# Performance work log

Hardware: AMD Instinct MI355X
Metric: run time of the kernel (lower is better)

Reference implementation:

```python
import jax, jax.numpy as jnp
import numpy as np

H, HD = 8, 32            # num_heads, head_dim
OUT = H * HD             # out_channels = 256
NUM_GRAPHS = 1


def segment_softmax(logits, seg, num_segments):
    m = jax.ops.segment_max(logits, seg, num_segments=num_segments)
    m = jnp.where(jnp.isfinite(m), m, 0.0)
    e = jnp.exp(logits - m[seg])
    s = jax.ops.segment_sum(e, seg, num_segments=num_segments)
    return e / (s[seg] + 1e-16)


def setup_inputs():
    key = jax.random.key(0)
    ks = jax.random.split(key, 16)
    N, E, IN = 30000, 600000, 128
    s = 0.05
    return {
        "x": jax.random.normal(ks[0], (N, IN), jnp.float32),
        "edge_index": jax.random.randint(ks[1], (2, E), 0, N, jnp.int32),
        "edge_attr": jax.random.normal(ks[2], (E,), jnp.float32),
        "batch": jnp.zeros((N,), jnp.int32),
        # per-head GATConv params (stacked over heads)
        "W": jax.random.normal(ks[3], (H, IN, HD), jnp.float32) * s,
        "a_src": jax.random.normal(ks[4], (H, HD), jnp.float32) * s,
        "a_dst": jax.random.normal(ks[5], (H, HD), jnp.float32) * s,
        "conv_b": jnp.zeros((H, HD), jnp.float32),
        # shared fc (used twice in forward)
        "fc_w": jax.random.normal(ks[6], (OUT, OUT), jnp.float32) * s,
        "fc_b": jnp.zeros((OUT,), jnp.float32),
        "ln_w": jnp.ones((OUT,), jnp.float32),
        "ln_b": jnp.zeros((OUT,), jnp.float32),
        "gate_w": jax.random.normal(ks[7], (1, OUT), jnp.float32) * s,
        "gate_b": jnp.zeros((1,), jnp.float32),
        "gfc_w": jax.random.normal(ks[8], (OUT, OUT), jnp.float32) * s,
        "gfc_b": jnp.zeros((OUT,), jnp.float32),
    }


def reference(x, edge_index, edge_attr, batch, W, a_src, a_dst, conv_b,
              fc_w, fc_b, ln_w, ln_b, gate_w, gate_b, gfc_w, gfc_b):
    N = x.shape[0]
    # (dropout p=0.2 is identity in eval mode)
    # --- multi-head GATConv (heads=1 each, vectorized over H); PyG default
    # add_self_loops=True; edge_dim=None so edge_attr is ignored by the conv.
    loops = jnp.arange(N, dtype=edge_index.dtype)
    src = jnp.concatenate([edge_index[0], loops])  # [Etot]
    dst = jnp.concatenate([edge_index[1], loops])
    xp = jnp.einsum('ni,hid->nhd', x, W)                    # [N,H,HD]
    alpha_src = jnp.sum(xp * a_src[None], axis=-1)          # [N,H]
    alpha_dst = jnp.sum(xp * a_dst[None], axis=-1)          # [N,H]
    logits = jax.nn.leaky_relu(alpha_src[src] + alpha_dst[dst], 0.2)  # [Etot,H]
    alpha = segment_softmax(logits, dst, N)                 # [Etot,H]
    msg = alpha[:, :, None] * xp[src]                        # [Etot,H,HD]
    out = jax.ops.segment_sum(msg, dst, num_segments=N) + conv_b[None]
    x_local = out.reshape(N, OUT)                            # concat over heads
    # --- dense re-attention / softmax fusion
    sa = jax.nn.softmax(jax.nn.leaky_relu(x_local @ fc_w.T + fc_b, 0.01), axis=-1)
    x_local = jax.nn.leaky_relu(x_local * sa, 0.2)
    x_local = x_local @ fc_w.T + fc_b
    # LayerNorm (eps=1e-5)
    mu = jnp.mean(x_local, axis=-1, keepdims=True)
    var = jnp.mean(jnp.square(x_local - mu), axis=-1, keepdims=True)
    x_local = (x_local - mu) / jnp.sqrt(var + 1e-5) * ln_w + ln_b
    # F.normalize(p=2, dim=1)
    nrm = jnp.sqrt(jnp.sum(jnp.square(x_local), axis=1, keepdims=True))
    x_local = x_local / jnp.maximum(nrm, 1e-12)
    # --- GlobalAttention pooling
    gate = (x_local @ gate_w.T + gate_b)[:, 0]               # [N]
    g = segment_softmax(gate, batch, NUM_GRAPHS)             # [N]
    x_global = jax.ops.segment_sum(g[:, None] * x_local, batch,
                                   num_segments=NUM_GRAPHS)  # [1,OUT]
    ga = jax.nn.softmax(jax.nn.relu(x_global @ gfc_w.T + gfc_b), axis=-1)
    return x_local * ga[batch]                               # [N,OUT]
```

## Files before the change

kernel.cpp:

```cpp
#include <hip/hip_runtime.h>


#define PAD 96

typedef __attribute__((ext_vector_type(8))) short bf16x8;
typedef __attribute__((ext_vector_type(4))) float f32x4;

__device__ __forceinline__ float leaky_f(float v, float s) { return v > 0.f ? v : s * v; }
__device__ __forceinline__ unsigned short f2bf(float f) {
  unsigned int u = __float_as_uint(f);
  u += 0x7fffu + ((u >> 16) & 1u);
  return (unsigned short)(u >> 16);
}
__device__ __forceinline__ float bf2f(unsigned short u) {
  return __uint_as_float(((unsigned int)u) << 16);
}
__device__ __forceinline__ float red16_sum(float v) {
#pragma unroll
  for (int m = 1; m < 16; m <<= 1) v += __shfl_xor(v, m);
  return v;
}
__device__ __forceinline__ float red16_max(float v) {
#pragma unroll
  for (int m = 1; m < 16; m <<= 1) v = fmaxf(v, __shfl_xor(v, m));
  return v;
}

__global__ void repack_zero_kernel(const float* __restrict__ W, const float* __restrict__ fc_w,
                                   const float* __restrict__ gfc_w,
                                   unsigned short* __restrict__ Wb,
                                   unsigned short* __restrict__ fcB, float* __restrict__ gfcT,
                                   int* __restrict__ count, int n) {
  int i = blockIdx.x * 256 + threadIdx.x;
  if (i < 256 * 128) {
    int c = i >> 7, k = i & 127;
    Wb[i] = f2bf(W[((c >> 5) * 128 + k) * 32 + (c & 31)]);
  } else if (i < 256 * 128 + 256 * 256) {
    int j = i - 256 * 128;
    fcB[j] = f2bf(fc_w[j]);
  } else if (i < 256 * 128 + 2 * 256 * 256) {
    int j = i - 256 * 128 - 256 * 256;
    gfcT[j] = gfc_w[(j & 255) * 256 + (j >> 8)];
  }
  if (i < n) count[i] = 0;
}

__global__ __launch_bounds__(256) void scatter_kernel(
    const int* __restrict__ esrc, const int* __restrict__ edst,
    int* __restrict__ count, int* __restrict__ ssrc, int E) {
  int base = (blockIdx.x * 256 + threadIdx.x) * 4;
  if (base + 4 <= E) {
    int4 d4 = *(const int4*)(edst + base);
    int4 s4 = *(const int4*)(esrc + base);
    int p0 = atomicAdd(&count[d4.x], 1);
    int p1 = atomicAdd(&count[d4.y], 1);
    int p2 = atomicAdd(&count[d4.z], 1);
    int p3 = atomicAdd(&count[d4.w], 1);
    if (p0 < PAD) ssrc[(size_t)d4.x * PAD + p0] = s4.x;
    if (p1 < PAD) ssrc[(size_t)d4.y * PAD + p1] = s4.y;
    if (p2 < PAD) ssrc[(size_t)d4.z * PAD + p2] = s4.z;
    if (p3 < PAD) ssrc[(size_t)d4.w * PAD + p3] = s4.w;
  } else {
    for (int i = base; i < E; ++i) {
      int d = edst[i];
      int p = atomicAdd(&count[d], 1);
      if (p < PAD) ssrc[(size_t)d * PAD + p] = esrc[i];
    }
  }
}

template <int A_BF16>
__device__ __forceinline__ void gemm_body_64x256(
    const void* __restrict__ Av, const unsigned short* __restrict__ B,
    int row0, int n_rows, int K, short As[64][72], short Bs[256][72],
    f32x4 acc[4][4]) {
  int t = threadIdx.x;
  int wave = t >> 6, lane = t & 63;
  int m16 = lane & 15, quad = lane >> 4;
  int wc = wave * 64;
  for (int k0 = 0; k0 < K; k0 += 64) {
    if (A_BF16) {
      const unsigned short* A = (const unsigned short*)Av;
#pragma unroll
      for (int p = 0; p < 2; ++p) {
        int e = (p * 256 + t) * 8;
        int row = e >> 6, k = e & 63;
        int ar = row0 + row; if (ar > n_rows - 1) ar = n_rows - 1;
        uint4 q = *(const uint4*)(A + (size_t)ar * K + k0 + k);
        *(uint4*)&As[row][k] = q;
      }
    } else {
      const float* A = (const float*)Av;
#pragma unroll
      for (int p = 0; p < 4; ++p) {
        int e = (p * 256 + t) * 4;
        int row = e >> 6, k = e & 63;
        int ar = row0 + row; if (ar > n_rows - 1) ar = n_rows - 1;
        float4 q = *(const float4*)(A + (size_t)ar * K + k0 + k);
        unsigned int lo = (unsigned int)f2bf(q.x) | ((unsigned int)f2bf(q.y) << 16);
        unsigned int hi = (unsigned int)f2bf(q.z) | ((unsigned int)f2bf(q.w) << 16);
        *(uint2*)&As[row][k] = make_uint2(lo, hi);
      }
    }
#pragma unroll
    for (int p = 0; p < 8; ++p) {
      int e = (p * 256 + t) * 8;
      int nn = e >> 6, k = e & 63;
      uint4 q = *(const uint4*)(B + (size_t)nn * K + k0 + k);
      *(uint4*)&Bs[nn][k] = q;
    }
    __syncthreads();
#pragma unroll
    for (int ks = 0; ks < 64; ks += 32) {
      bf16x8 af[4], bfr[4];
#pragma unroll
      for (int i = 0; i < 4; ++i)
        af[i] = *(const bf16x8*)&As[i * 16 + m16][ks + quad * 8];
#pragma unroll
      for (int j = 0; j < 4; ++j)
        bfr[j] = *(const bf16x8*)&Bs[wc + j * 16 + m16][ks + quad * 8];
#pragma unroll
      for (int i = 0; i < 4; ++i)
#pragma unroll
        for (int j = 0; j < 4; ++j)
          acc[i][j] = __builtin_amdgcn_mfma_f32_16x16x32_bf16(af[i], bfr[j], acc[i][j], 0, 0, 0);
    }
    __syncthreads();
  }
}

__global__ __launch_bounds__(256) void gemm_xp(
    const float* __restrict__ A, const unsigned short* __restrict__ B,
    const float* __restrict__ a_src, const float* __restrict__ a_dst,
    unsigned short* __restrict__ xpb, float* __restrict__ asrc,
    float* __restrict__ adst, int n_rows) {
  __shared__ short As[64][72];
  __shared__ short Bs[256][72];
  int t = threadIdx.x;
  int wave = t >> 6, lane = t & 63;
  int m16 = lane & 15, quad = lane >> 4;
  int wc = wave * 64;
  int row0 = blockIdx.x * 64;
  f32x4 acc[4][4];
#pragma unroll
  for (int i = 0; i < 4; ++i)
#pragma unroll
    for (int j = 0; j < 4; ++j) acc[i][j] = (f32x4){0.f, 0.f, 0.f, 0.f};
  gemm_body_64x256<0>(A, B, row0, n_rows, 128, As, Bs, acc);

  float av[4], bd[4];
#pragma unroll
  for (int j = 0; j < 4; ++j) {
    int c = wc + j * 16 + m16;
    av[j] = a_src[c];
    bd[j] = a_dst[c];
  }
#pragma unroll
  for (int i = 0; i < 4; ++i)
#pragma unroll
    for (int v = 0; v < 4; ++v) {
      int r = row0 + i * 16 + quad * 4 + v;
      if (r < n_rows) {
#pragma unroll
        for (int j = 0; j < 4; ++j)
          xpb[(size_t)r * 256 + wc + j * 16 + m16] = f2bf(acc[i][j][v]);
      }
      float s0 = acc[i][0][v] * av[0] + acc[i][1][v] * av[1];
      float s1 = acc[i][2][v] * av[2] + acc[i][3][v] * av[3];
      float d0 = acc[i][0][v] * bd[0] + acc[i][1][v] * bd[1];
      float d1 = acc[i][2][v] * bd[2] + acc[i][3][v] * bd[3];
      s0 = red16_sum(s0); s1 = red16_sum(s1);
      d0 = red16_sum(d0); d1 = red16_sum(d1);
      if (m16 == 0 && r < n_rows) {
        asrc[(size_t)r * 8 + 2 * wave] = s0;
        asrc[(size_t)r * 8 + 2 * wave + 1] = s1;
        adst[(size_t)r * 8 + 2 * wave] = d0;
        adst[(size_t)r * 8 + 2 * wave + 1] = d1;
      }
    }
}

__global__ __launch_bounds__(256) void gemm_sm(
    const float* __restrict__ A, const unsigned short* __restrict__ B,
    const float* __restrict__ bias, unsigned short* __restrict__ x2b, int n_rows) {
  __shared__ short As[64][72];
  __shared__ short Bs[256][72];
  __shared__ float red[4][64];
  __shared__ float rowv[64];
  int t = threadIdx.x;
  int wave = t >> 6, lane = t & 63;
  int m16 = lane & 15, quad = lane >> 4;
  int wc = wave * 64;
  int row0 = blockIdx.x * 64;
  f32x4 acc[4][4];
#pragma unroll
  for (int i = 0; i < 4; ++i)
#pragma unroll
    for (int j = 0; j < 4; ++j) acc[i][j] = (f32x4){0.f, 0.f, 0.f, 0.f};
  gemm_body_64x256<0>(A, B, row0, n_rows, 256, As, Bs, acc);

  float bvv[4];
#pragma unroll
  for (int j = 0; j < 4; ++j) bvv[j] = bias[wc + j * 16 + m16];
#pragma unroll
  for (int i = 0; i < 4; ++i)
#pragma unroll
    for (int j = 0; j < 4; ++j)
#pragma unroll
      for (int v = 0; v < 4; ++v)
        acc[i][j][v] = leaky_f(acc[i][j][v] + bvv[j], 0.01f);

  float M[4][4];
#pragma unroll
  for (int i = 0; i < 4; ++i)
#pragma unroll
    for (int v = 0; v < 4; ++v) {
      float m = fmaxf(fmaxf(acc[i][0][v], acc[i][1][v]), fmaxf(acc[i][2][v], acc[i][3][v]));
      M[i][v] = red16_max(m);
    }
  if (m16 == 0)
#pragma unroll
    for (int i = 0; i < 4; ++i)
#pragma unroll
      for (int v = 0; v < 4; ++v) red[wave][i * 16 + quad * 4 + v] = M[i][v];
  __syncthreads();
  if (t < 64) rowv[t] = fmaxf(fmaxf(red[0][t], red[1][t]), fmaxf(red[2][t], red[3][t]));
  __syncthreads();
#pragma unroll
  for (int i = 0; i < 4; ++i)
#pragma unroll
    for (int v = 0; v < 4; ++v) M[i][v] = rowv[i * 16 + quad * 4 + v];
  __syncthreads();

  float S[4][4];
#pragma unroll
  for (int i = 0; i < 4; ++i)
#pragma unroll
    for (int v = 0; v < 4; ++v) {
#pragma unroll
      for (int j = 0; j < 4; ++j) acc[i][j][v] = __expf(acc[i][j][v] - M[i][v]);
      float s = acc[i][0][v] + acc[i][1][v] + acc[i][2][v] + acc[i][3][v];
      S[i][v] = red16_sum(s);
    }
  if (m16 == 0)
#pragma unroll
    for (int i = 0; i < 4; ++i)
#pragma unroll
      for (int v = 0; v < 4; ++v) red[wave][i * 16 + quad * 4 + v] = S[i][v];
  __syncthreads();
  if (t < 64) rowv[t] = red[0][t] + red[1][t] + red[2][t] + red[3][t];
  __syncthreads();

#pragma unroll
  for (int i = 0; i < 4; ++i)
#pragma unroll
    for (int v = 0; v < 4; ++v) {
      int r = row0 + i * 16 + quad * 4 + v;
      float inv = 1.f / rowv[i * 16 + quad * 4 + v];
      if (r < n_rows) {
#pragma unroll
        for (int j = 0; j < 4; ++j) {
          int c = wc + j * 16 + m16;
          float xv = A[(size_t)r * 256 + c];
          x2b[(size_t)r * 256 + c] = f2bf(leaky_f(xv * acc[i][j][v] * inv, 0.2f));
        }
      }
    }
}

__global__ __launch_bounds__(256) void gemm_ln(
    const unsigned short* __restrict__ A, const unsigned short* __restrict__ B,
    const float* __restrict__ bias, const float* __restrict__ ln_w,
    const float* __restrict__ ln_b, const float* __restrict__ gate_w,
    const float* __restrict__ gate_b, unsigned short* __restrict__ Cout,
    float* __restrict__ pooled, float* __restrict__ pooledS, int n_rows) {
  __shared__ short As[64][72];
  __shared__ short Bs[256][72];
  __shared__ float red[4][64];
  __shared__ float rowv[64];
  __shared__ float eg[64];
  int t = threadIdx.x;
  int wave = t >> 6, lane = t & 63;
  int m16 = lane & 15, quad = lane >> 4;
  int wc = wave * 64;
  int row0 = blockIdx.x * 64;
  f32x4 acc[4][4];
#pragma unroll
  for (int i = 0; i < 4; ++i)
#pragma unroll
    for (int j = 0; j < 4; ++j) acc[i][j] = (f32x4){0.f, 0.f, 0.f, 0.f};
  gemm_body_64x256<1>(A, B, row0, n_rows, 256, As, Bs, acc);

  float bvv[4], lw[4], lb[4], gw[4];
#pragma unroll
  for (int j = 0; j < 4; ++j) {
    int c = wc + j * 16 + m16;
    bvv[j] = bias[c]; lw[j] = ln_w[c]; lb[j] = ln_b[c]; gw[j] = gate_w[c];
  }
#pragma unroll
  for (int i = 0; i < 4; ++i)
#pragma unroll
    for (int j = 0; j < 4; ++j)
#pragma unroll
      for (int v = 0; v < 4; ++v) acc[i][j][v] += bvv[j];

  float MU[4][4];
#pragma unroll
  for (int i = 0; i < 4; ++i)
#pragma unroll
    for (int v = 0; v < 4; ++v)
      MU[i][v] = red16_sum(acc[i][0][v] + acc[i][1][v] + acc[i][2][v] + acc[i][3][v]);
  if (m16 == 0)
#pragma unroll
    for (int i = 0; i < 4; ++i)
#pragma unroll
      for (int v = 0; v < 4; ++v) red[wave][i * 16 + quad * 4 + v] = MU[i][v];
  __syncthreads();
  if (t < 64) rowv[t] = (red[0][t] + red[1][t] + red[2][t] + red[3][t]) * (1.f / 256.f);
  __syncthreads();
#pragma unroll
  for (int i = 0; i < 4; ++i)
#pragma unroll
    for (int v = 0; v < 4; ++v) MU[i][v] = rowv[i * 16 + quad * 4 + v];
  __syncthreads();
#pragma unroll
  for (int i = 0; i < 4; ++i)
#pragma unroll
    for (int j = 0; j < 4; ++j)
#pragma unroll
      for (int v = 0; v < 4; ++v) acc[i][j][v] -= MU[i][v];

  float RS[4][4];
#pragma unroll
  for (int i = 0; i < 4; ++i)
#pragma unroll
    for (int v = 0; v < 4; ++v) {
      float q = acc[i][0][v] * acc[i][0][v] + acc[i][1][v] * acc[i][1][v] +
                acc[i][2][v] * acc[i][2][v] + acc[i][3][v] * acc[i][3][v];
      RS[i][v] = red16_sum(q);
    }
  if (m16 == 0)
#pragma unroll
    for (int i = 0; i < 4; ++i)
#pragma unroll
      for (int v = 0; v < 4; ++v) red[wave][i * 16 + quad * 4 + v] = RS[i][v];
  __syncthreads();
  if (t < 64)
    rowv[t] = rsqrtf((red[0][t] + red[1][t] + red[2][t] + red[3][t]) * (1.f / 256.f) + 1e-5f);
  __syncthreads();
#pragma unroll
  for (int i = 0; i < 4; ++i)
#pragma unroll
    for (int v = 0; v < 4; ++v) RS[i][v] = rowv[i * 16 + quad * 4 + v];
  __syncthreads();
#pragma unroll
  for (int i = 0; i < 4; ++i)
#pragma unroll
    for (int j = 0; j < 4; ++j)
#pragma unroll
      for (int v = 0; v < 4; ++v)
        acc[i][j][v] = acc[i][j][v] * RS[i][v] * lw[j] + lb[j];

  float NV[4][4];
#pragma unroll
  for (int i = 0; i < 4; ++i)
#pragma unroll
    for (int v = 0; v < 4; ++v) {
      float q = acc[i][0][v] * acc[i][0][v] + acc[i][1][v] * acc[i][1][v] +
                acc[i][2][v] * acc[i][2][v] + acc[i][3][v] * acc[i][3][v];
      NV[i][v] = red16_sum(q);
    }
  if (m16 == 0)
#pragma unroll
    for (int i = 0; i < 4; ++i)
#pragma unroll
      for (int v = 0; v < 4; ++v) red[wave][i * 16 + quad * 4 + v] = NV[i][v];
  __syncthreads();
  if (t < 64)
    rowv[t] = 1.f / fmaxf(sqrtf(red[0][t] + red[1][t] + red[2][t] + red[3][t]), 1e-12f);
  __syncthreads();
#pragma unroll
  for (int i = 0; i < 4; ++i)
#pragma unroll
    for (int v = 0; v < 4; ++v) NV[i][v] = rowv[i * 16 + quad * 4 + v];
  __syncthreads();
#pragma unroll
  for (int i = 0; i < 4; ++i)
#pragma unroll
    for (int j = 0; j < 4; ++j)
#pragma unroll
      for (int v = 0; v < 4; ++v) acc[i][j][v] *= NV[i][v];

  float GP[4][4];
#pragma unroll
  for (int i = 0; i < 4; ++i)
#pragma unroll
    for (int v = 0; v < 4; ++v) {
      float g = acc[i][0][v] * gw[0] + acc[i][1][v] * gw[1] +
                acc[i][2][v] * gw[2] + acc[i][3][v] * gw[3];
      GP[i][v] = red16_sum(g);
    }
  if (m16 == 0)
#pragma unroll
    for (int i = 0; i < 4; ++i)
#pragma unroll
      for (int v = 0; v < 4; ++v) red[wave][i * 16 + quad * 4 + v] = GP[i][v];
  __syncthreads();
  if (t < 64) {
    float gp = red[0][t] + red[1][t] + red[2][t] + red[3][t];
    float e = (row0 + t < n_rows) ? __expf(gp + gate_b[0]) : 0.f;
    eg[t] = e;
#pragma unroll
    for (int m = 1; m < 64; m <<= 1) e += __shfl_xor(e, m);
    if (t == 0) pooledS[blockIdx.x] = e;
  }
  __syncthreads();

  {
    float pt[4] = {0.f, 0.f, 0.f, 0.f};
#pragma unroll
    for (int i = 0; i < 4; ++i)
#pragma unroll
      for (int v = 0; v < 4; ++v) {
        float w = eg[i * 16 + quad * 4 + v];
#pragma unroll
        for (int j = 0; j < 4; ++j) pt[j] += w * acc[i][j][v];
      }
#pragma unroll
    for (int j = 0; j < 4; ++j) {
      float sj = pt[j];
      sj += __shfl_xor(sj, 16);
      sj += __shfl_xor(sj, 32);
      if (quad == 0) pooled[(size_t)blockIdx.x * 256 + wc + j * 16 + m16] = sj;
    }
  }

#pragma unroll
  for (int i = 0; i < 4; ++i)
#pragma unroll
    for (int v = 0; v < 4; ++v) {
      int r = row0 + i * 16 + quad * 4 + v;
      if (r < n_rows) {
#pragma unroll
        for (int j = 0; j < 4; ++j)
          Cout[(size_t)r * 256 + wc + j * 16 + m16] = f2bf(acc[i][j][v]);
      }
    }
}

__global__ __launch_bounds__(256) void agg_kernel(
    const unsigned short* __restrict__ xpb, const float* __restrict__ asrc,
    const float* __restrict__ adst, const int* __restrict__ count,
    const int* __restrict__ ssrc, const float4* __restrict__ conv_b4,
    float4* __restrict__ xloc4, int n_nodes) {
  int lane = threadIdx.x & 63, w = threadIdx.x >> 6;
  int n = blockIdx.x * 4 + w;
  if (n >= n_nodes) return;
  int h = lane >> 3;
  float ad = adst[n * 8 + h];
  float p = __expf(leaky_f(asrc[n * 8 + h] + ad, 0.2f));
  ushort4 xq = ((const ushort4*)(xpb + (size_t)n * 256))[lane];
  float4 acc;
  acc.x = p * bf2f(xq.x); acc.y = p * bf2f(xq.y);
  acc.z = p * bf2f(xq.z); acc.w = p * bf2f(xq.w);
  float ssum = p;
  int beg = n * PAD;
  int end = beg + count[n];
  int j = beg;
  for (; j + 8 <= end; j += 8) {
    int sv[8];
#pragma unroll
    for (int u = 0; u < 8; ++u) sv[u] = ssrc[j + u];
    float a[8];
#pragma unroll
    for (int u = 0; u < 8; ++u) a[u] = asrc[sv[u] * 8 + h];
    ushort4 q[8];
#pragma unroll
    for (int u = 0; u < 8; ++u) q[u] = ((const ushort4*)(xpb + (size_t)sv[u] * 256))[lane];
#pragma unroll
    for (int u = 0; u < 8; ++u) {
      float pu = __expf(leaky_f(a[u] + ad, 0.2f));
      acc.x += pu * bf2f(q[u].x); acc.y += pu * bf2f(q[u].y);
      acc.z += pu * bf2f(q[u].z); acc.w += pu * bf2f(q[u].w);
      ssum += pu;
    }
  }
  for (; j + 4 <= end; j += 4) {
    int sv0 = ssrc[j], sv1 = ssrc[j + 1], sv2 = ssrc[j + 2], sv3 = ssrc[j + 3];
    float a0 = asrc[sv0 * 8 + h];
    float a1 = asrc[sv1 * 8 + h];
    float a2 = asrc[sv2 * 8 + h];
    float a3 = asrc[sv3 * 8 + h];
    ushort4 q0 = ((const ushort4*)(xpb + (size_t)sv0 * 256))[lane];
    ushort4 q1 = ((const ushort4*)(xpb + (size_t)sv1 * 256))[lane];
    ushort4 q2 = ((const ushort4*)(xpb + (size_t)sv2 * 256))[lane];
    ushort4 q3 = ((const ushort4*)(xpb + (size_t)sv3 * 256))[lane];
    float p0 = __expf(leaky_f(a0 + ad, 0.2f));
    float p1 = __expf(leaky_f(a1 + ad, 0.2f));
    float p2 = __expf(leaky_f(a2 + ad, 0.2f));
    float p3 = __expf(leaky_f(a3 + ad, 0.2f));
    acc.x += p0 * bf2f(q0.x); acc.y += p0 * bf2f(q0.y);
    acc.z += p0 * bf2f(q0.z); acc.w += p0 * bf2f(q0.w);
    acc.x += p1 * bf2f(q1.x); acc.y += p1 * bf2f(q1.y);
    acc.z += p1 * bf2f(q1.z); acc.w += p1 * bf2f(q1.w);
    acc.x += p2 * bf2f(q2.x); acc.y += p2 * bf2f(q2.y);
    acc.z += p2 * bf2f(q2.z); acc.w += p2 * bf2f(q2.w);
    acc.x += p3 * bf2f(q3.x); acc.y += p3 * bf2f(q3.y);
    acc.z += p3 * bf2f(q3.z); acc.w += p3 * bf2f(q3.w);
    ssum += p0 + p1 + p2 + p3;
  }
  for (; j < end; ++j) {
    int sv = ssrc[j];
    float a1 = asrc[sv * 8 + h];
    ushort4 q = ((const ushort4*)(xpb + (size_t)sv * 256))[lane];
    float p1 = __expf(leaky_f(a1 + ad, 0.2f));
    acc.x += p1 * bf2f(q.x); acc.y += p1 * bf2f(q.y);
    acc.z += p1 * bf2f(q.z); acc.w += p1 * bf2f(q.w);
    ssum += p1;
  }
  float inv = 1.f / (ssum + 1e-16f);
  float4 b = conv_b4[lane];
  float4 o;
  o.x = acc.x * inv + b.x; o.y = acc.y * inv + b.y;
  o.z = acc.z * inv + b.z; o.w = acc.w * inv + b.w;
  xloc4[(size_t)n * 64 + lane] = o;
}

__global__ __launch_bounds__(1024) void finalize_gfc(
    const float* __restrict__ pooled, const float* __restrict__ pooledS, int nb,
    const float* __restrict__ gfcT, const float* __restrict__ gfc_b,
    float* __restrict__ ga) {
  __shared__ float sm[1024];
  __shared__ float xs[256];
  __shared__ float av[256];
  int t = threadIdx.x, c = t & 255, part = t >> 8;
  float s = 0.f;
  for (int b = t; b < nb; b += 1024) s += pooledS[b];
  sm[t] = s;
  __syncthreads();
  for (int st = 512; st > 0; st >>= 1) {
    if (t < st) sm[t] += sm[t + st];
    __syncthreads();
  }
  float S = sm[0];
  __syncthreads();
  float xc = 0.f;
#pragma unroll 4
  for (int b = part; b < nb; b += 4) xc += pooled[(size_t)b * 256 + c];
  sm[t] = xc;
  __syncthreads();
  if (part == 0) xs[c] = (sm[c] + sm[c + 256] + sm[c + 512] + sm[c + 768]) / (S + 1e-16f);
  __syncthreads();
  float a = 0.f;
  for (int i = part * 64; i < part * 64 + 64; ++i) a += xs[i] * gfcT[i * 256 + c];
  sm[t] = a;
  __syncthreads();
  if (part == 0)
    av[c] = fmaxf(sm[c] + sm[c + 256] + sm[c + 512] + sm[c + 768] + gfc_b[c], 0.f);
  __syncthreads();
  sm[t] = (t < 256) ? av[t] : -1e30f;
  __syncthreads();
  for (int st = 512; st > 0; st >>= 1) {
    if (t < st) sm[t] = fmaxf(sm[t], sm[t + st]);
    __syncthreads();
  }
  float m = sm[0];
  __syncthreads();
  if (part == 0) av[c] = __expf(av[c] - m);
  __syncthreads();
  sm[t] = (t < 256) ? av[t] : 0.f;
  __syncthreads();
  for (int st = 512; st > 0; st >>= 1) {
    if (t < st) sm[t] += sm[t + st];
    __syncthreads();
  }
  if (part == 0) ga[c] = av[c] / sm[0];
}

__global__ void out_kernel(const ushort4* __restrict__ xlb4, const float4* __restrict__ ga4,
                           float4* __restrict__ out4, int total4) {
  int i = blockIdx.x * 256 + threadIdx.x;
  if (i >= total4) return;
  ushort4 q = xlb4[i];
  float4 g = ga4[i & 63];
  float4 v;
  v.x = bf2f(q.x) * g.x; v.y = bf2f(q.y) * g.y;
  v.z = bf2f(q.z) * g.z; v.w = bf2f(q.w) * g.w;
  out4[i] = v;
}

extern "C" void kernel_launch(void* const* d_in, const int* in_sizes, int n_in,
                              void* d_out, int out_size, void* d_ws, size_t ws_size,
                              hipStream_t stream) {
  const float* x      = (const float*)d_in[0];
  const int* edge_idx = (const int*)d_in[1];
  const float* W      = (const float*)d_in[4];
  const float* a_src  = (const float*)d_in[5];
  const float* a_dst  = (const float*)d_in[6];
  const float* conv_b = (const float*)d_in[7];
  const float* fc_w   = (const float*)d_in[8];
  const float* fc_b   = (const float*)d_in[9];
  const float* ln_w   = (const float*)d_in[10];
  const float* ln_b   = (const float*)d_in[11];
  const float* gate_w = (const float*)d_in[12];
  const float* gate_b = (const float*)d_in[13];
  const float* gfc_w  = (const float*)d_in[14];
  const float* gfc_b  = (const float*)d_in[15];
  (void)n_in; (void)out_size; (void)ws_size;

  int N = in_sizes[0] / 128;
  int E = in_sizes[1] / 2;
  const int* src = edge_idx;
  const int* dst = edge_idx + E;

  char* p = (char*)d_ws;
  auto alloc = [&](size_t bytes) -> char* {
    char* r = p;
    p += (bytes + 255) & ~(size_t)255;
    return r;
  };
  int g64 = (N + 63) / 64;
  float*          xloc = (float*)alloc((size_t)N * 256 * 4);
  unsigned short* xpb  = (unsigned short*)alloc((size_t)N * 256 * 2);
  unsigned short* x2b  = (unsigned short*)alloc((size_t)N * 256 * 2);
  unsigned short* xlb  = (unsigned short*)alloc((size_t)N * 256 * 2);
  float* asrc  = (float*)alloc((size_t)N * 8 * 4);
  float* adst  = (float*)alloc((size_t)N * 8 * 4);
  unsigned short* Wb   = (unsigned short*)alloc(256 * 128 * 2);
  unsigned short* fcB  = (unsigned short*)alloc(256 * 256 * 2);
  float* gfcT  = (float*)alloc(256 * 256 * 4);
  int*   count = (int*)alloc((size_t)N * 4);
  int*   ssrc  = (int*)alloc((size_t)N * PAD * 4);
  float* pooled  = (float*)alloc((size_t)g64 * 256 * 4);
  float* pooledS = (float*)alloc((size_t)g64 * 4);
  float* ga    = (float*)alloc(1024);

  repack_zero_kernel<<<(256 * 128 + 2 * 256 * 256 + 255) / 256, 256, 0, stream>>>(
      W, fc_w, gfc_w, Wb, fcB, gfcT, count, N);
  scatter_kernel<<<(E + 1023) / 1024, 256, 0, stream>>>(src, dst, count, ssrc, E);
  gemm_xp<<<g64, 256, 0, stream>>>(x, Wb, a_src, a_dst, xpb, asrc, adst, N);
  agg_kernel<<<(N + 3) / 4, 256, 0, stream>>>(
      xpb, asrc, adst, count, ssrc, (const float4*)conv_b, (float4*)xloc, N);
  gemm_sm<<<g64, 256, 0, stream>>>(xloc, fcB, fc_b, x2b, N);
  gemm_ln<<<g64, 256, 0, stream>>>(x2b, fcB, fc_b, ln_w, ln_b, gate_w, gate_b,
                                   xlb, pooled, pooledS, N);
  finalize_gfc<<<1, 1024, 0, stream>>>(pooled, pooledS, g64, gfcT, gfc_b, ga);
  out_kernel<<<(N * 64 + 255) / 256, 256, 0, stream>>>(
      (const ushort4*)xlb, (const float4*)ga, (float4*)d_out, N * 64);
}
```

Baseline: 257.2 us.

## Fuse edge scatter into xp GEMM launch, halve-wave aggregation with bf16 output

The edge CSR scatter now runs as extra blocks inside the xp GEMM launch, removing one kernel launch and letting the two phases overlap. The aggregation kernel is rewritten so each half-wave handles one node with 16-byte gathers. Attention exponentials are computed once per (edge, head) and shared across lanes with shuffles. The aggregated features are written as bf16 instead of fp32, and gemm_sm reads them through its bf16 path. This cuts write and read traffic but adds rounding error before the fc GEMM and softmax product.

```diff
diff --git a/kernel.cpp b/kernel.cpp
--- a/kernel.cpp
+++ b/kernel.cpp
@@ -14,6 +14,12 @@
 }
 __device__ __forceinline__ float bf2f(unsigned short u) {
   return __uint_as_float(((unsigned int)u) << 16);
+}
+__device__ __forceinline__ float bf_lo(unsigned int u) {
+  return __uint_as_float(u << 16);
+}
+__device__ __forceinline__ float bf_hi(unsigned int u) {
+  return __uint_as_float(u & 0xffff0000u);
 }
 __device__ __forceinline__ float red16_sum(float v) {
 #pragma unroll
@@ -45,30 +51,6 @@
   if (i < n) count[i] = 0;
 }
 
-__global__ __launch_bounds__(256) void scatter_kernel(
-    const int* __restrict__ esrc, const int* __restrict__ edst,
-    int* __restrict__ count, int* __restrict__ ssrc, int E) {
-  int base = (blockIdx.x * 256 + threadIdx.x) * 4;
-  if (base + 4 <= E) {
-    int4 d4 = *(const int4*)(edst + base);
-    int4 s4 = *(const int4*)(esrc + base);
-    int p0 = atomicAdd(&count[d4.x], 1);
-    int p1 = atomicAdd(&count[d4.y], 1);
-    int p2 = atomicAdd(&count[d4.z], 1);
-    int p3 = atomicAdd(&count[d4.w], 1);
-    if (p0 < PAD) ssrc[(size_t)d4.x * PAD + p0] = s4.x;
-    if (p1 < PAD) ssrc[(size_t)d4.y * PAD + p1] = s4.y;
-    if (p2 < PAD) ssrc[(size_t)d4.z * PAD + p2] = s4.z;
-    if (p3 < PAD) ssrc[(size_t)d4.w * PAD + p3] = s4.w;
-  } else {
-    for (int i = base; i < E; ++i) {
-      int d = edst[i];
-      int p = atomicAdd(&count[d], 1);
-      if (p < PAD) ssrc[(size_t)d * PAD + p] = esrc[i];
-    }
-  }
-}
-
 template <int A_BF16>
 __device__ __forceinline__ void gemm_body_64x256(
     const void* __restrict__ Av, const unsigned short* __restrict__ B,
@@ -129,13 +111,37 @@
   }
 }
 
-__global__ __launch_bounds__(256) void gemm_xp(
+__global__ __launch_bounds__(256) void gemm_xp_scatter(
     const float* __restrict__ A, const unsigned short* __restrict__ B,
     const float* __restrict__ a_src, const float* __restrict__ a_dst,
     unsigned short* __restrict__ xpb, float* __restrict__ asrc,
-    float* __restrict__ adst, int n_rows) {
+    float* __restrict__ adst, int n_rows,
+    const int* __restrict__ esrc, const int* __restrict__ edst,
+    int* __restrict__ count, int* __restrict__ ssrc, int E, int gemm_blocks) {
   __shared__ short As[64][72];
   __shared__ short Bs[256][72];
+  if ((int)blockIdx.x >= gemm_blocks) {
+    int base = (((int)blockIdx.x - gemm_blocks) * 256 + threadIdx.x) * 4;
+    if (base + 4 <= E) {
+      int4 d4 = *(const int4*)(edst + base);
+      int4 s4 = *(const int4*)(esrc + base);
+      int p0 = atomicAdd(&count[d4.x], 1);
+      int p1 = atomicAdd(&count[d4.y], 1);
+      int p2 = atomicAdd(&count[d4.z], 1);
+      int p3 = atomicAdd(&count[d4.w], 1);
+      if (p0 < PAD) ssrc[(size_t)d4.x * PAD + p0] = s4.x;
+      if (p1 < PAD) ssrc[(size_t)d4.y * PAD + p1] = s4.y;
+      if (p2 < PAD) ssrc[(size_t)d4.z * PAD + p2] = s4.z;
+      if (p3 < PAD) ssrc[(size_t)d4.w * PAD + p3] = s4.w;
+    } else {
+      for (int i = base; i < E; ++i) {
+        int d = edst[i];
+        int p = atomicAdd(&count[d], 1);
+        if (p < PAD) ssrc[(size_t)d * PAD + p] = esrc[i];
+      }
+    }
+    return;
+  }
   int t = threadIdx.x;
   int wave = t >> 6, lane = t & 63;
   int m16 = lane & 15, quad = lane >> 4;
@@ -180,8 +186,96 @@
     }
 }
 
+__global__ __launch_bounds__(256) void agg_kernel(
+    const unsigned short* __restrict__ xpb, const float* __restrict__ asrc,
+    const float* __restrict__ adst, const int* __restrict__ count,
+    const int* __restrict__ ssrc, const float* __restrict__ conv_b,
+    unsigned short* __restrict__ xlocb, int n_nodes) {
+  int t = threadIdx.x;
+  int lane = t & 63;
+  int hl = lane & 31;
+  int half = lane >> 5;
+  int wv = t >> 6;
+  int n = blockIdx.x * 8 + wv * 2 + half;
+  bool active = n < n_nodes;
+  int nn = active ? n : 0;
+  int hc = hl >> 2;
+  int hp = hl & 7;
+  int up = hl >> 3;
+  int srcbase = (half << 5) + hc;
+
+  float ad_p = adst[nn * 8 + hp];
+  float ad_c = adst[nn * 8 + hc];
+
+  float p = __expf(leaky_f(asrc[nn * 8 + hc] + ad_c, 0.2f));
+  uint4 q = *(const uint4*)(xpb + (size_t)nn * 256 + hl * 8);
+  float acc[8];
+  acc[0] = p * bf_lo(q.x); acc[1] = p * bf_hi(q.x);
+  acc[2] = p * bf_lo(q.y); acc[3] = p * bf_hi(q.y);
+  acc[4] = p * bf_lo(q.z); acc[5] = p * bf_hi(q.z);
+  acc[6] = p * bf_lo(q.w); acc[7] = p * bf_hi(q.w);
+  float ssum = p;
+
+  int beg = nn * PAD;
+  int end = beg + (active ? count[nn] : 0);
+  int j = beg;
+  for (; j + 4 <= end; j += 4) {
+    int4 s4 = *(const int4*)(ssrc + j);
+    int svp = (up & 1) ? ((up & 2) ? s4.w : s4.y) : ((up & 2) ? s4.z : s4.x);
+    float pp = __expf(leaky_f(asrc[svp * 8 + hp] + ad_p, 0.2f));
+    uint4 q0 = *(const uint4*)(xpb + (size_t)s4.x * 256 + hl * 8);
+    uint4 q1 = *(const uint4*)(xpb + (size_t)s4.y * 256 + hl * 8);
+    uint4 q2 = *(const uint4*)(xpb + (size_t)s4.z * 256 + hl * 8);
+    uint4 q3 = *(const uint4*)(xpb + (size_t)s4.w * 256 + hl * 8);
+    float p0 = __shfl(pp, srcbase);
+    float p1 = __shfl(pp, srcbase + 8);
+    float p2 = __shfl(pp, srcbase + 16);
+    float p3 = __shfl(pp, srcbase + 24);
+    acc[0] += p0 * bf_lo(q0.x); acc[1] += p0 * bf_hi(q0.x);
+    acc[2] += p0 * bf_lo(q0.y); acc[3] += p0 * bf_hi(q0.y);
+    acc[4] += p0 * bf_lo(q0.z); acc[5] += p0 * bf_hi(q0.z);
+    acc[6] += p0 * bf_lo(q0.w); acc[7] += p0 * bf_hi(q0.w);
+    acc[0] += p1 * bf_lo(q1.x); acc[1] += p1 * bf_hi(q1.x);
+    acc[2] += p1 * bf_lo(q1.y); acc[3] += p1 * bf_hi(q1.y);
+    acc[4] += p1 * bf_lo(q1.z); acc[5] += p1 * bf_hi(q1.z);
+    acc[6] += p1 * bf_lo(q1.w); acc[7] += p1 * bf_hi(q1.w);
+    acc[0] += p2 * bf_lo(q2.x); acc[1] += p2 * bf_hi(q2.x);
+    acc[2] += p2 * bf_lo(q2.y); acc[3] += p2 * bf_hi(q2.y);
+    acc[4] += p2 * bf_lo(q2.z); acc[5] += p2 * bf_hi(q2.z);
+    acc[6] += p2 * bf_lo(q2.w); acc[7] += p2 * bf_hi(q2.w);
+    acc[0] += p3 * bf_lo(q3.x); acc[1] += p3 * bf_hi(q3.x);
+    acc[2] += p3 * bf_lo(q3.y); acc[3] += p3 * bf_hi(q3.y);
+    acc[4] += p3 * bf_lo(q3.z); acc[5] += p3 * bf_hi(q3.z);
+    acc[6] += p3 * bf_lo(q3.w); acc[7] += p3 * bf_hi(q3.w);
+    ssum += p0 + p1 + p2 + p3;
+  }
+  for (; j < end; ++j) {
+    int sv = ssrc[j];
+    float p1 = __expf(leaky_f(asrc[sv * 8 + hc] + ad_c, 0.2f));
+    uint4 q1 = *(const uint4*)(xpb + (size_t)sv * 256 + hl * 8);
+    acc[0] += p1 * bf_lo(q1.x); acc[1] += p1 * bf_hi(q1.x);
+    acc[2] += p1 * bf_lo(q1.y); acc[3] += p1 * bf_hi(q1.y);
+    acc[4] += p1 * bf_lo(q1.z); acc[5] += p1 * bf_hi(q1.z);
+    acc[6] += p1 * bf_lo(q1.w); acc[7] += p1 * bf_hi(q1.w);
+    ssum += p1;
+  }
+  if (!active) return;
+  float inv = 1.f / (ssum + 1e-16f);
+  float4 b0 = *(const float4*)(conv_b + hl * 8);
+  float4 b1 = *(const float4*)(conv_b + hl * 8 + 4);
+  unsigned int w0 = (unsigned int)f2bf(acc[0] * inv + b0.x) |
+                    ((unsigned int)f2bf(acc[1] * inv + b0.y) << 16);
+  unsigned int w1 = (unsigned int)f2bf(acc[2] * inv + b0.z) |
+                    ((unsigned int)f2bf(acc[3] * inv + b0.w) << 16);
+  unsigned int w2 = (unsigned int)f2bf(acc[4] * inv + b1.x) |
+                    ((unsigned int)f2bf(acc[5] * inv + b1.y) << 16);
+  unsigned int w3 = (unsigned int)f2bf(acc[6] * inv + b1.z) |
+                    ((unsigned int)f2bf(acc[7] * inv + b1.w) << 16);
+  *(uint4*)(xlocb + (size_t)n * 256 + hl * 8) = make_uint4(w0, w1, w2, w3);
+}
+
 __global__ __launch_bounds__(256) void gemm_sm(
-    const float* __restrict__ A, const unsigned short* __restrict__ B,
+    const unsigned short* __restrict__ A, const unsigned short* __restrict__ B,
     const float* __restrict__ bias, unsigned short* __restrict__ x2b, int n_rows) {
   __shared__ short As[64][72];
   __shared__ short Bs[256][72];
@@ -197,7 +291,7 @@
   for (int i = 0; i < 4; ++i)
 #pragma unroll
     for (int j = 0; j < 4; ++j) acc[i][j] = (f32x4){0.f, 0.f, 0.f, 0.f};
-  gemm_body_64x256<0>(A, B, row0, n_rows, 256, As, Bs, acc);
+  gemm_body_64x256<1>(A, B, row0, n_rows, 256, As, Bs, acc);
 
   float bvv[4];
 #pragma unroll
@@ -261,7 +355,7 @@
 #pragma unroll
         for (int j = 0; j < 4; ++j) {
           int c = wc + j * 16 + m16;
-          float xv = A[(size_t)r * 256 + c];
+          float xv = bf2f(A[(size_t)r * 256 + c]);
           x2b[(size_t)r * 256 + c] = f2bf(leaky_f(xv * acc[i][j][v] * inv, 0.2f));
         }
       }
@@ -446,84 +540,6 @@
           Cout[(size_t)r * 256 + wc + j * 16 + m16] = f2bf(acc[i][j][v]);
       }
     }
-}
-
-__global__ __launch_bounds__(256) void agg_kernel(
-    const unsigned short* __restrict__ xpb, const float* __restrict__ asrc,
-    const float* __restrict__ adst, const int* __restrict__ count,
-    const int* __restrict__ ssrc, const float4* __restrict__ conv_b4,
-    float4* __restrict__ xloc4, int n_nodes) {
-  int lane = threadIdx.x & 63, w = threadIdx.x >> 6;
-  int n = blockIdx.x * 4 + w;
-  if (n >= n_nodes) return;
-  int h = lane >> 3;
-  float ad = adst[n * 8 + h];
-  float p = __expf(leaky_f(asrc[n * 8 + h] + ad, 0.2f));
-  ushort4 xq = ((const ushort4*)(xpb + (size_t)n * 256))[lane];
-  float4 acc;
-  acc.x = p * bf2f(xq.x); acc.y = p * bf2f(xq.y);
-  acc.z = p * bf2f(xq.z); acc.w = p * bf2f(xq.w);
-  float ssum = p;
-  int beg = n * PAD;
-  int end = beg + count[n];
-  int j = beg;
-  for (; j + 8 <= end; j += 8) {
-    int sv[8];
-#pragma unroll
-    for (int u = 0; u < 8; ++u) sv[u] = ssrc[j + u];
-    float a[8];
-#pragma unroll
-    for (int u = 0; u < 8; ++u) a[u] = asrc[sv[u] * 8 + h];
-    ushort4 q[8];
-#pragma unroll
-    for (int u = 0; u < 8; ++u) q[u] = ((const ushort4*)(xpb + (size_t)sv[u] * 256))[lane];
-#pragma unroll
-    for (int u = 0; u < 8; ++u) {
-      float pu = __expf(leaky_f(a[u] + ad, 0.2f));
-      acc.x += pu * bf2f(q[u].x); acc.y += pu * bf2f(q[u].y);
-      acc.z += pu * bf2f(q[u].z); acc.w += pu * bf2f(q[u].w);
-      ssum += pu;
-    }
-  }
-  for (; j + 4 <= end; j += 4) {
-    int sv0 = ssrc[j], sv1 = ssrc[j + 1], sv2 = ssrc[j + 2], sv3 = ssrc[j + 3];
-    float a0 = asrc[sv0 * 8 + h];
-    float a1 = asrc[sv1 * 8 + h];
-    float a2 = asrc[sv2 * 8 + h];
-    float a3 = asrc[sv3 * 8 + h];
-    ushort4 q0 = ((const ushort4*)(xpb + (size_t)sv0 * 256))[lane];
-    ushort4 q1 = ((const ushort4*)(xpb + (size_t)sv1 * 256))[lane];
-    ushort4 q2 = ((const ushort4*)(xpb + (size_t)sv2 * 256))[lane];
-    ushort4 q3 = ((const ushort4*)(xpb + (size_t)sv3 * 256))[lane];
-    float p0 = __expf(leaky_f(a0 + ad, 0.2f));
-    float p1 = __expf(leaky_f(a1 + ad, 0.2f));
-    float p2 = __expf(leaky_f(a2 + ad, 0.2f));
-    float p3 = __expf(leaky_f(a3 + ad, 0.2f));
-    acc.x += p0 * bf2f(q0.x); acc.y += p0 * bf2f(q0.y);
-    acc.z += p0 * bf2f(q0.z); acc.w += p0 * bf2f(q0.w);
-    acc.x += p1 * bf2f(q1.x); acc.y += p1 * bf2f(q1.y);
-    acc.z += p1 * bf2f(q1.z); acc.w += p1 * bf2f(q1.w);
-    acc.x += p2 * bf2f(q2.x); acc.y += p2 * bf2f(q2.y);
-    acc.z += p2 * bf2f(q2.z); acc.w += p2 * bf2f(q2.w);
-    acc.x += p3 * bf2f(q3.x); acc.y += p3 * bf2f(q3.y);
-    acc.z += p3 * bf2f(q3.z); acc.w += p3 * bf2f(q3.w);
-    ssum += p0 + p1 + p2 + p3;
-  }
-  for (; j < end; ++j) {
-    int sv = ssrc[j];
-    float a1 = asrc[sv * 8 + h];
-    ushort4 q = ((const ushort4*)(xpb + (size_t)sv * 256))[lane];
-    float p1 = __expf(leaky_f(a1 + ad, 0.2f));
-    acc.x += p1 * bf2f(q.x); acc.y += p1 * bf2f(q.y);
-    acc.z += p1 * bf2f(q.z); acc.w += p1 * bf2f(q.w);
-    ssum += p1;
-  }
-  float inv = 1.f / (ssum + 1e-16f);
-  float4 b = conv_b4[lane];
-  float4 o;
-  o.x = acc.x * inv + b.x; o.y = acc.y * inv + b.y;
-  o.z = acc.z * inv + b.z; o.w = acc.w * inv + b.w;
-  xloc4[(size_t)n * 64 + lane] = o;
 }
 
 __global__ __launch_bounds__(1024) void finalize_gfc(
@@ -620,7 +636,7 @@
     return r;
   };
   int g64 = (N + 63) / 64;
-  float*          xloc = (float*)alloc((size_t)N * 256 * 4);
+  unsigned short* xlocb = (unsigned short*)alloc((size_t)N * 256 * 2);
   unsigned short* xpb  = (unsigned short*)alloc((size_t)N * 256 * 2);
   unsigned short* x2b  = (unsigned short*)alloc((size_t)N * 256 * 2);
   unsigned short* xlb  = (unsigned short*)alloc((size_t)N * 256 * 2);
@@ -635,13 +651,15 @@
   float* pooledS = (float*)alloc((size_t)g64 * 4);
   float* ga    = (float*)alloc(1024);
 
+  int eb4 = (E + 1023) / 1024;
+
   repack_zero_kernel<<<(256 * 128 + 2 * 256 * 256 + 255) / 256, 256, 0, stream>>>(
       W, fc_w, gfc_w, Wb, fcB, gfcT, count, N);
-  scatter_kernel<<<(E + 1023) / 1024, 256, 0, stream>>>(src, dst, count, ssrc, E);
-  gemm_xp<<<g64, 256, 0, stream>>>(x, Wb, a_src, a_dst, xpb, asrc, adst, N);
-  agg_kernel<<<(N + 3) / 4, 256, 0, stream>>>(
-      xpb, asrc, adst, count, ssrc, (const float4*)conv_b, (float4*)xloc, N);
-  gemm_sm<<<g64, 256, 0, stream>>>(xloc, fcB, fc_b, x2b, N);
+  gemm_xp_scatter<<<g64 + eb4, 256, 0, stream>>>(
+      x, Wb, a_src, a_dst, xpb, asrc, adst, N, src, dst, count, ssrc, E, g64);
+  agg_kernel<<<(N + 7) / 8, 256, 0, stream>>>(
+      xpb, asrc, adst, count, ssrc, conv_b, xlocb, N);
+  gemm_sm<<<g64, 256, 0, stream>>>(xlocb, fcB, fc_b, x2b, N);
   gemm_ln<<<g64, 256, 0, stream>>>(x2b, fcB, fc_b, ln_w, ln_b, gate_w, gate_b,
                                    xlb, pooled, pooledS, N);
   finalize_gfc<<<1, 1024, 0, stream>>>(pooled, pooledS, g64, gfcT, gfc_b, ga);
```

After: 255.5 us. No clear change (-0.6%).
